# Kernel tuning notes

Measured on AMD Instinct MI355X. Metric: run time of the kernel, lower is better.

The kernel has to match this reference:

```python
import jax, jax.numpy as jnp
import numpy as np

B, T, D = 2, 2048, 1024
H, HD = 16, 64           # num_heads, head_dim (key_dim = value_dim = H*HD = D)
K = 4                    # short conv kernel size
EPS = 1e-6


def setup_inputs() -> dict:
    key = jax.random.key(0)
    ks = jax.random.split(key, 16)
    w = lambda k, shape, s=0.02: jax.random.normal(k, shape, jnp.float32) * s
    dt = jnp.exp(jax.random.uniform(ks[12], (H,)) * (np.log(0.1) - np.log(0.001)) + np.log(0.001))
    dt = jnp.clip(dt, 0.0001, None)
    return {
        "hidden_states": jax.random.normal(ks[0], (B, T, D), jnp.float32),
        "Wq": w(ks[1], (H * HD, D)),
        "Wk": w(ks[2], (H * HD, D)),
        "Wv": w(ks[3], (H * HD, D)),
        "Wa": w(ks[4], (H, D)),
        "Wb": w(ks[5], (H, D)),
        "Wg": w(ks[6], (H * HD, D)),
        "Wo": w(ks[7], (D, H * HD)),
        "q_norm_w": jnp.ones((HD,), jnp.float32),
        "k_norm_w": jnp.ones((HD,), jnp.float32),
        "o_norm_w": jnp.ones((HD,), jnp.float32),
        "A_log": jnp.log(jax.random.uniform(ks[11], (H,), jnp.float32, 0.5, 8.0)),
        "dt_bias": dt + jnp.log(-jnp.expm1(-dt)),
        "conv_q_w": w(ks[13], (H * HD, K), 0.2),
        "conv_k_w": w(ks[14], (H * HD, K), 0.2),
        "conv_v_w": w(ks[15], (H * HD, K), 0.2),
    }


def _short_conv_silu(x, w):
    # causal depthwise conv1d (kernel K) + SiLU; x: [B,T,C], w: [C,K]
    xc = jnp.transpose(x, (0, 2, 1))                       # [B,C,T]
    y = jax.lax.conv_general_dilated(
        xc, w[:, None, :], (1,), [(w.shape[-1] - 1, 0)],
        dimension_numbers=("NCH", "OIH", "NCH"), feature_group_count=w.shape[0])
    y = jnp.transpose(y, (0, 2, 1))
    return y * jax.nn.sigmoid(y)


def _rmsnorm(x, w):
    return x * jax.lax.rsqrt(jnp.mean(x * x, -1, keepdims=True) + EPS) * w


def _l2norm(x):
    return x * jax.lax.rsqrt(jnp.sum(x * x, -1, keepdims=True) + EPS)


def _forward(hidden_states, Wq, Wk, Wv, Wa, Wb, Wg, Wo,
             q_norm_w, k_norm_w, o_norm_w, A_log, dt_bias,
             conv_q_w, conv_k_w, conv_v_w):
    h = hidden_states
    q = _short_conv_silu(h @ Wq.T, conv_q_w).reshape(B, T, H, HD)
    k = _short_conv_silu(h @ Wk.T, conv_k_w).reshape(B, T, H, HD)
    v = _short_conv_silu(h @ Wv.T, conv_v_w).reshape(B, T, H, HD)
    q = _l2norm(_rmsnorm(q, q_norm_w))
    k = _l2norm(_rmsnorm(k, k_norm_w))
    beta = jax.nn.sigmoid(h @ Wb.T)                                  # [B,T,H]
    g = -jnp.exp(A_log) * jax.nn.softplus(h @ Wa.T + dt_bias)        # [B,T,H]
    scale = HD ** -0.5

    def step(S, inp):  # S: [B,H,dk,dv]
        qt, kt, vt, gt, bt = inp
        S = S * jnp.exp(gt)[:, :, None, None]
        kv = jnp.einsum("bhk,bhkv->bhv", kt, S)
        delta = (vt - kv) * bt[..., None]
        S = S + jnp.einsum("bhk,bhv->bhkv", kt, delta)
        o = jnp.einsum("bhk,bhkv->bhv", qt * scale, S)
        return S, o

    tm = lambda x: jnp.swapaxes(x, 0, 1)  # [B,T,...] -> [T,B,...]
    S0 = jnp.zeros((B, H, HD, HD), jnp.float32)
    _, o = jax.lax.scan(step, S0, (tm(q), tm(k), tm(v), tm(g), tm(beta)))
    o = jnp.swapaxes(o, 0, 1)                                        # [B,T,H,HD]

    gv = (h @ Wg.T).reshape(B, T, H, HD)
    o = _rmsnorm(o, o_norm_w) * (gv * jax.nn.sigmoid(gv))            # swish gate
    return o.reshape(B, T, H * HD) @ Wo.T


def reference(hidden_states, Wq, Wk, Wv, Wa, Wb, Wg, Wo,
              q_norm_w, k_norm_w, o_norm_w, A_log, dt_bias,
              conv_q_w, conv_k_w, conv_v_w):
    return _forward(hidden_states, Wq, Wk, Wv, Wa, Wb, Wg, Wo,
                    q_norm_w, k_norm_w, o_norm_w, A_log, dt_bias,
                    conv_q_w, conv_k_w, conv_v_w)
```

## Files before the change

### kernel.cpp

```cpp
#include <hip/hip_runtime.h>
#include <cstdint>
#include <cstddef>

#define B_ 2
#define T_ 2048
#define D_ 1024
#define H_ 16
#define HD_ 64
#define NC_ 32

typedef unsigned short u16;
typedef __attribute__((ext_vector_type(8))) short bf16x8;
typedef __attribute__((ext_vector_type(4))) float f32x4;

__device__ __forceinline__ float dot4(float4 a, float4 b, float acc) {
  return fmaf(a.x, b.x, fmaf(a.y, b.y, fmaf(a.z, b.z, fmaf(a.w, b.w, acc))));
}
__device__ __forceinline__ u16 f2bf(float f) {
  unsigned u = __float_as_uint(f);
  u += 0x7fffu + ((u >> 16) & 1u);
  return (u16)(u >> 16);
}
__device__ __forceinline__ float bf2f(u16 v) {
  return __uint_as_float(((unsigned)v) << 16);
}
__device__ __forceinline__ float4 ld4bf(const u16* p) {
  uint2 v = *(const uint2*)p;
  return float4{__uint_as_float(v.x << 16),
                __uint_as_float(v.x & 0xffff0000u),
                __uint_as_float(v.y << 16),
                __uint_as_float(v.y & 0xffff0000u)};
}
__device__ __forceinline__ bf16x8 pack8(float4 a, float4 b) {
  union { u16 us[8]; bf16x8 v; } p;
  p.us[0] = f2bf(a.x); p.us[1] = f2bf(a.y); p.us[2] = f2bf(a.z); p.us[3] = f2bf(a.w);
  p.us[4] = f2bf(b.x); p.us[5] = f2bf(b.y); p.us[6] = f2bf(b.z); p.us[7] = f2bf(b.w);
  return p.v;
}
__device__ __forceinline__ void glds16(const u16* g, u16* l) {
  __builtin_amdgcn_global_load_lds(
      (const __attribute__((address_space(1))) void*)g,
      (__attribute__((address_space(3))) void*)l, 16, 0, 0);
}
__device__ __forceinline__ float4 conv4(float4 x0, float4 x1, float4 x2, float4 x3,
                                        const float4* w) {
  float4 y;
  y.x = fmaf(w[0].x, x0.x, fmaf(w[0].y, x1.x, fmaf(w[0].z, x2.x, w[0].w * x3.x)));
  y.y = fmaf(w[1].x, x0.y, fmaf(w[1].y, x1.y, fmaf(w[1].z, x2.y, w[1].w * x3.y)));
  y.z = fmaf(w[2].x, x0.z, fmaf(w[2].y, x1.z, fmaf(w[2].z, x2.z, w[2].w * x3.z)));
  y.w = fmaf(w[3].x, x0.w, fmaf(w[3].y, x1.w, fmaf(w[3].z, x2.w, w[3].w * x3.w)));
  return y;
}
__device__ __forceinline__ float4 silu4(float4 a) {
  return float4{a.x / (1.f + __expf(-a.x)), a.y / (1.f + __expf(-a.y)),
                a.z / (1.f + __expf(-a.z)), a.w / (1.f + __expf(-a.w))};
}

__global__ __launch_bounds__(256) void cvt_all(
    const float* __restrict__ h, const float* __restrict__ w0,
    const float* __restrict__ w1, const float* __restrict__ w2,
    const float* __restrict__ w3, const float* __restrict__ w4,
    u16* __restrict__ h_bf, u16* __restrict__ wb)
{
  const int blk = blockIdx.x;
  const float* src;
  u16* dst;
  int lb;
  if (blk < 2048) { src = h; dst = h_bf; lb = blk; }
  else {
    int k = (blk - 2048) >> 9, r = (blk - 2048) & 511;
    src = k == 0 ? w0 : k == 1 ? w1 : k == 2 ? w2 : k == 3 ? w3 : w4;
    dst = wb + (size_t)k * 1048576;
    lb = r;
  }
  int i = (lb * 256 + threadIdx.x) * 8;
  float4 v0 = *(const float4*)(src + i);
  float4 v1 = *(const float4*)(src + i + 4);
  union { u16 us[8]; uint4 u4; } p;
  p.us[0] = f2bf(v0.x); p.us[1] = f2bf(v0.y); p.us[2] = f2bf(v0.z); p.us[3] = f2bf(v0.w);
  p.us[4] = f2bf(v1.x); p.us[5] = f2bf(v1.y); p.us[6] = f2bf(v1.z); p.us[7] = f2bf(v1.w);
  *(uint4*)(dst + i) = p.u4;
}

__global__ __launch_bounds__(512, 1) void gemm_bf16_4(const u16* __restrict__ A,
    const u16* __restrict__ W0, const u16* __restrict__ W1,
    const u16* __restrict__ W2, const u16* __restrict__ W3,
    u16* __restrict__ C0, u16* __restrict__ C1,
    u16* __restrict__ C2, u16* __restrict__ C3)
{
  __shared__ u16 As[3 * 256 * 32];
  __shared__ u16 Bs[3 * 256 * 32];
  const int K = 1024, N = 1024;
  const int sel = blockIdx.y >> 2;
  const u16* Bw = sel == 0 ? W0 : sel == 1 ? W1 : sel == 2 ? W2 : W3;
  u16* C = sel == 0 ? C0 : sel == 1 ? C1 : sel == 2 ? C2 : C3;
  const int row0 = blockIdx.x * 256;
  const int col0 = (blockIdx.y & 3) * 256;
  const int tid = threadIdx.x;
  const int lane = tid & 63, wave = tid >> 6;
  const int wm = wave >> 2, wn = wave & 3;
  const int lr = lane & 15, lkq = lane >> 4;
  const int lkp = (lkq ^ ((lr >> 1) & 3)) * 8;

  f32x4 acc[8][4];
  #pragma unroll
  for (int i = 0; i < 8; ++i)
    #pragma unroll
    for (int j = 0; j < 4; ++j) acc[i][j] = f32x4{0.f, 0.f, 0.f, 0.f};

  auto STAGE = [&](int buf, int kt) {
    u16* ab = As + buf * 8192;
    u16* bb = Bs + buf * 8192;
    #pragma unroll
    for (int g = 0; g < 2; ++g) {
      const int idx = g * 512 + tid;
      const int rr = idx >> 2, cl = idx & 3;
      const int csw = (cl ^ ((rr >> 1) & 3)) * 8;
      glds16(A  + (size_t)(row0 + rr) * K + kt * 32 + csw, ab + idx * 8);
      glds16(Bw + (size_t)(col0 + rr) * K + kt * 32 + csw, bb + idx * 8);
    }
  };

  const int KT = K >> 5;
  STAGE(0, 0); STAGE(1, 1); STAGE(2, 2);
  asm volatile("s_waitcnt vmcnt(8)" ::: "memory");
  __builtin_amdgcn_s_barrier();
  __builtin_amdgcn_sched_barrier(0);

  for (int kt = 0; kt < KT; ++kt) {
    const int cur = kt % 3;
    const u16* Asc = As + cur * 8192;
    const u16* Bsc = Bs + cur * 8192;
    bf16x8 af[8], bfr[4];
    #pragma unroll
    for (int i = 0; i < 8; ++i)
      af[i] = *(const bf16x8*)&Asc[(wm * 128 + i * 16 + lr) * 32 + lkp];
    #pragma unroll
    for (int j = 0; j < 4; ++j)
      bfr[j] = *(const bf16x8*)&Bsc[(wn * 64 + j * 16 + lr) * 32 + lkp];
    __builtin_amdgcn_s_setprio(1);
    #pragma unroll
    for (int i = 0; i < 4; ++i)
      #pragma unroll
      for (int j = 0; j < 4; ++j)
        acc[i][j] = __builtin_amdgcn_mfma_f32_16x16x32_bf16(af[i], bfr[j], acc[i][j], 0, 0, 0);
    __builtin_amdgcn_s_setprio(0);
    asm volatile("s_waitcnt lgkmcnt(0)" ::: "memory");
    __builtin_amdgcn_sched_barrier(0);
    __builtin_amdgcn_s_barrier();
    __builtin_amdgcn_sched_barrier(0);
    if (kt + 3 < KT) {
      STAGE(cur, kt + 3);
      asm volatile("s_waitcnt vmcnt(4)" ::: "memory");
    } else {
      asm volatile("s_waitcnt vmcnt(0)" ::: "memory");
    }
    __builtin_amdgcn_s_setprio(1);
    #pragma unroll
    for (int i = 4; i < 8; ++i)
      #pragma unroll
      for (int j = 0; j < 4; ++j)
        acc[i][j] = __builtin_amdgcn_mfma_f32_16x16x32_bf16(af[i], bfr[j], acc[i][j], 0, 0, 0);
    __builtin_amdgcn_s_setprio(0);
    __builtin_amdgcn_sched_barrier(0);
    __builtin_amdgcn_s_barrier();
    __builtin_amdgcn_sched_barrier(0);
  }

  const int orow = row0 + wm * 128 + (lane >> 4) * 4;
  const int ocol = col0 + wn * 64 + lr;
  #pragma unroll
  for (int i = 0; i < 8; ++i)
    #pragma unroll
    for (int j = 0; j < 4; ++j)
      #pragma unroll
      for (int r = 0; r < 4; ++r)
        C[(size_t)(orow + i * 16 + r) * N + ocol + j * 16] = f2bf(acc[i][j][r]);
}

__device__ __forceinline__ void gemm_core128(const u16* __restrict__ A,
    const u16* __restrict__ Bw, float* __restrict__ C,
    u16* As, u16* Bs, int row0, int col0, int K, int N)
{
  const int tid = threadIdx.x;
  const int lane = tid & 63, wave = tid >> 6;
  const int wr = (wave >> 1) * 64, wc = (wave & 1) * 64;
  const int lr = lane & 15;
  const int lkp = (((lane >> 4) ^ ((lr >> 1) & 3))) * 8;
  const int rql = (lane >> 2);
  const int cql = (((lane & 3) ^ ((rql >> 1) & 3))) * 8;
  const u16* gA0 = A + (size_t)(row0 + wave * 16 + rql) * K + cql;
  const u16* gA1 = A + (size_t)(row0 + (wave + 4) * 16 + rql) * K + cql;
  const u16* gB0 = Bw + (size_t)(col0 + wave * 16 + rql) * K + cql;
  const u16* gB1 = Bw + (size_t)(col0 + (wave + 4) * 16 + rql) * K + cql;

  f32x4 acc[4][4];
  #pragma unroll
  for (int i = 0; i < 4; ++i)
    #pragma unroll
    for (int j = 0; j < 4; ++j) acc[i][j] = f32x4{0.f, 0.f, 0.f, 0.f};

  auto STAGE = [&](int buf, int kt) {
    u16* ab = As + buf * 4096;
    u16* bb = Bs + buf * 4096;
    glds16(gA0 + kt * 32, ab + wave * 512);
    glds16(gA1 + kt * 32, ab + (wave + 4) * 512);
    glds16(gB0 + kt * 32, bb + wave * 512);
    glds16(gB1 + kt * 32, bb + (wave + 4) * 512);
  };

  const int KT = K >> 5;
  STAGE(0, 0);
  STAGE(1, 1);
  int cur = 0;
  for (int kt = 0; kt < KT; ++kt) {
    if (kt + 2 < KT) {
      STAGE(cur == 0 ? 2 : (cur == 1 ? 0 : 1), kt + 2);
      asm volatile("s_waitcnt vmcnt(8)" ::: "memory");
    } else if (kt + 1 < KT) {
      asm volatile("s_waitcnt vmcnt(4)" ::: "memory");
    } else {
      asm volatile("s_waitcnt vmcnt(0)" ::: "memory");
    }
    __builtin_amdgcn_s_barrier();
    __builtin_amdgcn_sched_barrier(0);
    const u16* Asc = As + cur * 4096;
    const u16* Bsc = Bs + cur * 4096;
    bf16x8 af[4], bf[4];
    #pragma unroll
    for (int i = 0; i < 4; ++i) af[i] = *(const bf16x8*)&Asc[(wr + i * 16 + lr) * 32 + lkp];
    #pragma unroll
    for (int j = 0; j < 4; ++j) bf[j] = *(const bf16x8*)&Bsc[(wc + j * 16 + lr) * 32 + lkp];
    #pragma unroll
    for (int i = 0; i < 4; ++i)
      #pragma unroll
      for (int j = 0; j < 4; ++j)
        acc[i][j] = __builtin_amdgcn_mfma_f32_16x16x32_bf16(af[i], bf[j], acc[i][j], 0, 0, 0);
    __builtin_amdgcn_sched_barrier(0);
    __builtin_amdgcn_s_barrier();
    cur = (cur == 2) ? 0 : cur + 1;
  }
  const int orow = row0 + wr + (lane >> 4) * 4;
  const int ocol = col0 + wc + lr;
  #pragma unroll
  for (int i = 0; i < 4; ++i)
    #pragma unroll
    for (int j = 0; j < 4; ++j)
      #pragma unroll
      for (int r = 0; r < 4; ++r)
        C[(size_t)(orow + i * 16 + r) * N + ocol + j * 16] = acc[i][j][r];
}

__global__ __launch_bounds__(256) void gemm_bf16_1(const u16* __restrict__ A,
    const u16* __restrict__ Bw, float* __restrict__ C)
{
  __shared__ u16 As[3 * 128 * 32];
  __shared__ u16 Bs[3 * 128 * 32];
  gemm_core128(A, Bw, C, As, Bs, blockIdx.x * 128, blockIdx.y * 128, 1024, 1024);
}

#define SPW 261
__global__ __launch_bounds__(256) void smallproj(const float* __restrict__ Hs,
    const float* __restrict__ Wa, const float* __restrict__ Wb,
    const float* __restrict__ Alog, const float* __restrict__ dtb,
    float* __restrict__ Gout, float* __restrict__ Bout)
{
  __shared__ float hT[16][SPW];
  __shared__ float wT[32][SPW];
  const int row0 = blockIdx.x * 16;
  const int tid = threadIdx.x;
  const int r = tid >> 5;
  const int c = tid & 31;
  float a0 = 0.f, a1 = 0.f;
  for (int kc = 0; kc < 4; ++kc) {
    const int k0 = kc * 256;
    #pragma unroll
    for (int i = 0; i < 4; ++i) {
      int e4 = tid + i * 256;
      int rr = e4 >> 6, k4 = (e4 & 63) * 4;
      *(float4*)&hT[rr][k4] = *(const float4*)&Hs[(size_t)(row0 + rr) * D_ + k0 + k4];
    }
    #pragma unroll
    for (int i = 0; i < 8; ++i) {
      int e4 = tid + i * 256;
      int rr = e4 >> 6, k4 = (e4 & 63) * 4;
      const float* wsrc = (rr < 16) ? (Wa + (size_t)rr * D_) : (Wb + (size_t)(rr - 16) * D_);
      *(float4*)&wT[rr][k4] = *(const float4*)&wsrc[k0 + k4];
    }
    __syncthreads();
    #pragma unroll 8
    for (int k = 0; k < 256; k += 4) {
      float4 wv = *(const float4*)&wT[c][k];
      float4 h0 = *(const float4*)&hT[r][k];
      float4 h1 = *(const float4*)&hT[r + 8][k];
      a0 = dot4(h0, wv, a0);
      a1 = dot4(h1, wv, a1);
    }
    __syncthreads();
  }
  if (c < 16) {
    const float al = -__expf(Alog[c]);
    const float db = dtb[c];
    float x0 = a0 + db, x1 = a1 + db;
    float sp0 = fmaxf(x0, 0.f) + log1pf(__expf(-fabsf(x0)));
    float sp1 = fmaxf(x1, 0.f) + log1pf(__expf(-fabsf(x1)));
    Gout[(size_t)(row0 + r) * H_ + c] = al * sp0;
    Gout[(size_t)(row0 + r + 8) * H_ + c] = al * sp1;
  } else {
    const int hd = c - 16;
    Bout[(size_t)(row0 + r) * H_ + hd] = 1.f / (1.f + __expf(-a0));
    Bout[(size_t)(row0 + r + 8) * H_ + hd] = 1.f / (1.f + __expf(-a1));
  }
}

__global__ __launch_bounds__(256) void p1_chunk(
    const u16* __restrict__ Kp, const u16* __restrict__ Vp,
    const float* __restrict__ Gg, const float* __restrict__ Bb,
    const float* __restrict__ ckw, const float* __restrict__ cvw,
    const float* __restrict__ knw,
    u16* __restrict__ Ubf, u16* __restrict__ Wbf, u16* __restrict__ Kcb,
    float* __restrict__ Gcum, float* __restrict__ Mbuf, float* __restrict__ Nbuf)
{
  __shared__ u16 Kbf[64][72];
  __shared__ float Am[64][68];
  __shared__ float XT[128][68];
  __shared__ float gc[64], bet[64];
  const int bhc = blockIdx.x;
  const int bh = bhc >> 5, c = bhc & 31;
  const int b = bh >> 4, h = bh & 15;
  const int tid = threadIdx.x;
  const int lane = tid & 63, wave = tid >> 6;
  const int lr = lane & 15, lkq = lane >> 4;
  const size_t rowbase = ((size_t)b*T_ + c*64)*H_ + h;
  const int c4 = (tid & 15) * 4;
  const int hh64 = h * 64;

  if (tid < 64) {
    float gv = Gg[rowbase + (size_t)tid*H_];
    #pragma unroll
    for (int off = 1; off < 64; off <<= 1) {
      float up = __shfl_up(gv, off, 64);
      if (tid >= off) gv += up;
    }
    gc[tid] = gv;
    Gcum[(size_t)bhc*64 + tid] = gv;
    bet[tid] = Bb[rowbase + (size_t)tid*H_];
  }

  {
    float4 wk[4];
    float nwv[4];
    #pragma unroll
    for (int cc = 0; cc < 4; ++cc) {
      wk[cc] = *(const float4*)(ckw + (hh64 + c4 + cc) * 4);
      nwv[cc] = knw[c4 + cc];
    }
    #pragma unroll
    for (int k = 0; k < 4; ++k) {
      const int t = (tid >> 4) + k * 16;
      const int gt = c * 64 + t;
      const u16* src = Kp + (rowbase + (size_t)t * H_) * 64 + c4;
      float4 x3 = ld4bf(src);
      float4 x2 = (gt >= 1) ? ld4bf(src - D_)   : float4{0,0,0,0};
      float4 x1 = (gt >= 2) ? ld4bf(src - 2*D_) : float4{0,0,0,0};
      float4 x0 = (gt >= 3) ? ld4bf(src - 3*D_) : float4{0,0,0,0};
      float4 y = silu4(conv4(x0, x1, x2, x3, wk));
      float ss = fmaf(y.x, y.x, fmaf(y.y, y.y, fmaf(y.z, y.z, y.w * y.w)));
      ss += __shfl_xor(ss, 1); ss += __shfl_xor(ss, 2);
      ss += __shfl_xor(ss, 4); ss += __shfl_xor(ss, 8);
      const float inv1 = rsqrtf(ss * (1.f/64.f) + 1e-6f);
      float4 z = {y.x*inv1*nwv[0], y.y*inv1*nwv[1], y.z*inv1*nwv[2], y.w*inv1*nwv[3]};
      float s2 = fmaf(z.x, z.x, fmaf(z.y, z.y, fmaf(z.z, z.z, z.w * z.w)));
      s2 += __shfl_xor(s2, 1); s2 += __shfl_xor(s2, 2);
      s2 += __shfl_xor(s2, 4); s2 += __shfl_xor(s2, 8);
      const float inv2 = rsqrtf(s2 + 1e-6f);
      u16 tmp[4] = {f2bf(z.x*inv2), f2bf(z.y*inv2), f2bf(z.z*inv2), f2bf(z.w*inv2)};
      *(uint2*)&Kbf[t][c4] = *(uint2*)tmp;
      *(uint2*)&Kcb[(size_t)bhc*4096 + (size_t)t*64 + c4] = *(uint2*)tmp;
    }
  }
  __syncthreads();

  {
    bf16x8 afA[2];
    #pragma unroll
    for (int ks = 0; ks < 2; ++ks)
      afA[ks] = *(const bf16x8*)&Kbf[16*wave + lr][ks*32 + lkq*8];
    __builtin_amdgcn_s_setprio(1);
    #pragma unroll
    for (int j = 0; j < 4; ++j) {
      f32x4 accA = f32x4{0.f, 0.f, 0.f, 0.f};
      #pragma unroll
      for (int ks = 0; ks < 2; ++ks) {
        bf16x8 bfr = *(const bf16x8*)&Kbf[16*j + lr][ks*32 + lkq*8];
        accA = __builtin_amdgcn_mfma_f32_16x16x32_bf16(afA[ks], bfr, accA, 0, 0, 0);
      }
      const int s = 16*j + lr;
      #pragma unroll
      for (int r = 0; r < 4; ++r) {
        int t = 16*wave + lkq*4 + r;
        Am[t][s] = (s < t) ? bet[t] * __expf(gc[t] - gc[s]) * accA[r] : 0.f;
      }
    }
    __builtin_amdgcn_s_setprio(0);
  }
  {
    float4 wv[4];
    #pragma unroll
    for (int cc = 0; cc < 4; ++cc)
      wv[cc] = *(const float4*)(cvw + (hh64 + c4 + cc) * 4);
    #pragma unroll
    for (int k = 0; k < 4; ++k) {
      const int t = (tid >> 4) + k * 16;
      const int gt = c * 64 + t;
      const u16* src = Vp + (rowbase + (size_t)t * H_) * 64 + c4;
      float4 x3 = ld4bf(src);
      float4 x2 = (gt >= 1) ? ld4bf(src - D_)   : float4{0,0,0,0};
      float4 x1 = (gt >= 2) ? ld4bf(src - 2*D_) : float4{0,0,0,0};
      float4 x0 = (gt >= 3) ? ld4bf(src - 3*D_) : float4{0,0,0,0};
      float4 vv = silu4(conv4(x0, x1, x2, x3, wv));
      const float bt = bet[t];
      const float ek = bt * __expf(gc[t]);
      XT[c4+0][t] = bt * vv.x; XT[c4+1][t] = bt * vv.y;
      XT[c4+2][t] = bt * vv.z; XT[c4+3][t] = bt * vv.w;
      XT[64+c4+0][t] = ek * bf2f(Kbf[t][c4+0]);
      XT[64+c4+1][t] = ek * bf2f(Kbf[t][c4+1]);
      XT[64+c4+2][t] = ek * bf2f(Kbf[t][c4+2]);
      XT[64+c4+3][t] = ek * bf2f(Kbf[t][c4+3]);
    }
  }
  __syncthreads();

  for (int st = 0; st < 4; ++st) {
    if (st > 0) {
      const int nks = (st == 3) ? 2 : 1;
      f32x4 accU0 = f32x4{0.f,0.f,0.f,0.f}, accU1 = f32x4{0.f,0.f,0.f,0.f};
      __builtin_amdgcn_s_setprio(1);
      for (int ks = 0; ks < nks; ++ks) {
        const int m0 = ks*32 + lkq*8;
        bf16x8 af;
        if (m0 + 8 <= 16*st) {
          float4 a0 = *(const float4*)&Am[16*st + lr][m0];
          float4 a1 = *(const float4*)&Am[16*st + lr][m0 + 4];
          af = pack8(a0, a1);
        } else {
          af = bf16x8{0,0,0,0,0,0,0,0};
        }
        {
          const int cb = (wave*2 + 0) * 16;
          float4 b0 = *(const float4*)&XT[cb + lr][m0];
          float4 b1 = *(const float4*)&XT[cb + lr][m0 + 4];
          accU0 = __builtin_amdgcn_mfma_f32_16x16x32_bf16(af, pack8(b0, b1), accU0, 0, 0, 0);
        }
        {
          const int cb = (wave*2 + 1) * 16;
          float4 b0 = *(const float4*)&XT[cb + lr][m0];
          float4 b1 = *(const float4*)&XT[cb + lr][m0 + 4];
          accU1 = __builtin_amdgcn_mfma_f32_16x16x32_bf16(af, pack8(b0, b1), accU1, 0, 0, 0);
        }
      }
      __builtin_amdgcn_s_setprio(0);
      #pragma unroll
      for (int r = 0; r < 4; ++r) {
        const int t = 16*st + lkq*4 + r;
        XT[(wave*2+0)*16 + lr][t] -= accU0[r];
        XT[(wave*2+1)*16 + lr][t] -= accU1[r];
      }
      __syncthreads();
    }
    if (tid < 128) {
      const int bs = 16*st;
      float x[16];
      #pragma unroll
      for (int q = 0; q < 4; ++q)
        *(float4*)&x[q*4] = *(const float4*)&XT[tid][bs + q*4];
      #pragma unroll
      for (int tau = 1; tau < 16; ++tau) {
        float a = 0.f, a2 = 0.f;
        #pragma unroll
        for (int m = 0; m < tau; m += 2) {
          a = fmaf(Am[bs+tau][bs+m], x[m], a);
          if (m + 1 < tau) a2 = fmaf(Am[bs+tau][bs+m+1], x[m+1], a2);
        }
        x[tau] -= (a + a2);
      }
      #pragma unroll
      for (int q = 0; q < 4; ++q)
        *(float4*)&XT[tid][bs + q*4] = *(const float4*)&x[q*4];
    }
    __syncthreads();
  }

  for (int e = tid; e < 4096; e += 256) {
    int t = e >> 6, j = e & 63;
    Ubf[(size_t)bhc*4096 + e] = f2bf(XT[j][t]);
    Wbf[(size_t)bhc*4096 + e] = f2bf(XT[64+j][t]);
  }

  u16* KTb = (u16*)&Am[0][0];
  if (tid < 64) bet[tid] = __expf(gc[63] - gc[tid]);
  __syncthreads();
  for (int e4 = tid; e4 < 1024; e4 += 256) {
    int t = e4 >> 4, a4 = (e4 & 15) * 4;
    u16 k0 = Kbf[t][a4+0], k1 = Kbf[t][a4+1], k2 = Kbf[t][a4+2], k3 = Kbf[t][a4+3];
    KTb[(a4+0)*72 + t] = k0;
    KTb[(a4+1)*72 + t] = k1;
    KTb[(a4+2)*72 + t] = k2;
    KTb[(a4+3)*72 + t] = k3;
  }
  __syncthreads();

  bf16x8 afK[2];
  #pragma unroll
  for (int ks = 0; ks < 2; ++ks)
    afK[ks] = *(const bf16x8*)&KTb[(16*wave + lr)*72 + ks*32 + lkq*8];
  const float bC = __expf(gc[63]);
  const size_t ob = (size_t)bhc * 4096;
  #pragma unroll
  for (int j = 0; j < 4; ++j) {
    f32x4 aM = f32x4{0.f,0.f,0.f,0.f}, aN = f32x4{0.f,0.f,0.f,0.f};
    __builtin_amdgcn_s_setprio(1);
    #pragma unroll
    for (int ks = 0; ks < 2; ++ks) {
      const int m0 = ks*32 + lkq*8;
      float4 sc0 = *(const float4*)&bet[m0];
      float4 sc1 = *(const float4*)&bet[m0 + 4];
      float4 w0 = *(const float4*)&XT[64 + 16*j + lr][m0];
      float4 w1 = *(const float4*)&XT[64 + 16*j + lr][m0 + 4];
      float4 u0 = *(const float4*)&XT[16*j + lr][m0];
      float4 u1 = *(const float4*)&XT[16*j + lr][m0 + 4];
      w0.x*=sc0.x; w0.y*=sc0.y; w0.z*=sc0.z; w0.w*=sc0.w;
      w1.x*=sc1.x; w1.y*=sc1.y; w1.z*=sc1.z; w1.w*=sc1.w;
      u0.x*=sc0.x; u0.y*=sc0.y; u0.z*=sc0.z; u0.w*=sc0.w;
      u1.x*=sc1.x; u1.y*=sc1.y; u1.z*=sc1.z; u1.w*=sc1.w;
      aM = __builtin_amdgcn_mfma_f32_16x16x32_bf16(afK[ks], pack8(w0, w1), aM, 0, 0, 0);
      aN = __builtin_amdgcn_mfma_f32_16x16x32_bf16(afK[ks], pack8(u0, u1), aN, 0, 0, 0);
    }
    __builtin_amdgcn_s_setprio(0);
    const int cc = 16*j + lr;
    #pragma unroll
    for (int r = 0; r < 4; ++r) {
      const int a = 16*wave + lkq*4 + r;
      Mbuf[ob + (size_t)a*64 + cc] = (a == cc ? bC : 0.f) - aM[r];
      Nbuf[ob + (size_t)a*64 + cc] = aN[r];
    }
  }
}

__global__ __launch_bounds__(256) void pscanA(float* __restrict__ Mbuf,
    float* __restrict__ Nbuf)
{
  __shared__ float OM[2][64][68];
  __shared__ float ON[2][64][68];
  __shared__ float NM[2][64][68];
  const int blk = blockIdx.x;
  const int bh = blk >> 3, g = blk & 7;
  const size_t s0 = ((size_t)bh * 32 + g * 4) * 4096;
  const int tid = threadIdx.x;
  const int p0 = (tid >> 4) * 4;
  const int q0 = (tid & 15) * 4;
  for (int e4 = tid; e4 < 1024; e4 += 256) {
    int r = e4 >> 4, c4 = (e4 & 15) * 4;
    *(float4*)&OM[0][r][c4] = *(const float4*)&Mbuf[s0 + (size_t)r*64 + c4];
    *(float4*)&ON[0][r][c4] = *(const float4*)&Nbuf[s0 + (size_t)r*64 + c4];
    *(float4*)&NM[0][r][c4] = *(const float4*)&Mbuf[s0 + 4096 + (size_t)r*64 + c4];
  }
  __syncthreads();
  for (int s = 0; s < 3; ++s) {
    const int cur = s & 1, nxt = cur ^ 1;
    const size_t wslot = s0 + (size_t)(s + 1) * 4096;
    if (s < 2) {
      for (int e4 = tid; e4 < 1024; e4 += 256) {
        int r = e4 >> 4, c4 = (e4 & 15) * 4;
        *(float4*)&NM[nxt][r][c4] = *(const float4*)&Mbuf[wslot + 4096 + (size_t)r*64 + c4];
      }
    }
    float aM[4][4], aN[4][4];
    #pragma unroll
    for (int r = 0; r < 4; ++r) {
      float4 nv = *(const float4*)&Nbuf[wslot + (size_t)(p0+r)*64 + q0];
      aM[r][0]=0.f; aM[r][1]=0.f; aM[r][2]=0.f; aM[r][3]=0.f;
      aN[r][0]=nv.x; aN[r][1]=nv.y; aN[r][2]=nv.z; aN[r][3]=nv.w;
    }
    for (int m4 = 0; m4 < 64; m4 += 4) {
      float xv[4][4];
      #pragma unroll
      for (int r = 0; r < 4; ++r) {
        float4 v = *(const float4*)&NM[cur][p0+r][m4];
        xv[r][0]=v.x; xv[r][1]=v.y; xv[r][2]=v.z; xv[r][3]=v.w;
      }
      #pragma unroll
      for (int mm = 0; mm < 4; ++mm) {
        float4 ym = *(const float4*)&OM[cur][m4+mm][q0];
        float4 yn = *(const float4*)&ON[cur][m4+mm][q0];
        #pragma unroll
        for (int r = 0; r < 4; ++r) {
          aM[r][0] = fmaf(xv[r][mm], ym.x, aM[r][0]);
          aM[r][1] = fmaf(xv[r][mm], ym.y, aM[r][1]);
          aM[r][2] = fmaf(xv[r][mm], ym.z, aM[r][2]);
          aM[r][3] = fmaf(xv[r][mm], ym.w, aM[r][3]);
          aN[r][0] = fmaf(xv[r][mm], yn.x, aN[r][0]);
          aN[r][1] = fmaf(xv[r][mm], yn.y, aN[r][1]);
          aN[r][2] = fmaf(xv[r][mm], yn.z, aN[r][2]);
          aN[r][3] = fmaf(xv[r][mm], yn.w, aN[r][3]);
        }
      }
    }
    #pragma unroll
    for (int r = 0; r < 4; ++r) {
      float4 vm = {aM[r][0], aM[r][1], aM[r][2], aM[r][3]};
      float4 vn = {aN[r][0], aN[r][1], aN[r][2], aN[r][3]};
      *(float4*)&Mbuf[wslot + (size_t)(p0+r)*64 + q0] = vm;
      *(float4*)&Nbuf[wslot + (size_t)(p0+r)*64 + q0] = vn;
      *(float4*)&OM[nxt][p0+r][q0] = vm;
      *(float4*)&ON[nxt][p0+r][q0] = vn;
    }
    __syncthreads();
  }
}

__global__ __launch_bounds__(256) void pscanB(const float* __restrict__ Mbuf,
    const float* __restrict__ Nbuf, float* __restrict__ S0b)
{
  __shared__ float ST[2][64][68];
  __shared__ float MT[64][68];
  const int bh = blockIdx.x;
  const size_t base = (size_t)bh * 32 * 4096;
  const int tid = threadIdx.x;
  const int j0 = (tid >> 4) * 4, a0 = tid & 15;
  for (int e4 = tid; e4 < 1024; e4 += 256) {
    int r = e4 >> 4, c4 = (e4 & 15) * 4;
    *(float4*)&ST[0][r][c4] = float4{0.f, 0.f, 0.f, 0.f};
    *(float4*)&S0b[base + (size_t)r*64 + c4] = float4{0.f, 0.f, 0.f, 0.f};
  }
  for (int g = 0; g < 7; ++g) {
    const int cur = g & 1, nxt = cur ^ 1;
    const size_t tslot = base + (size_t)(4*g + 3) * 4096;
    for (int e4 = tid; e4 < 1024; e4 += 256) {
      int r = e4 >> 4, c4 = (e4 & 15) * 4;
      *(float4*)&MT[r][c4] = *(const float4*)&Mbuf[tslot + (size_t)r*64 + c4];
    }
    float acc[4][4];
    #pragma unroll
    for (int r = 0; r < 4; ++r)
      #pragma unroll
      for (int s = 0; s < 4; ++s)
        acc[r][s] = Nbuf[tslot + (size_t)(a0 + 16*s)*64 + j0 + r];
    __syncthreads();
    for (int k4 = 0; k4 < 64; k4 += 4) {
      float4 xr[4];
      #pragma unroll
      for (int r = 0; r < 4; ++r) xr[r] = *(const float4*)&ST[cur][j0+r][k4];
      #pragma unroll
      for (int s = 0; s < 4; ++s) {
        float4 yv = *(const float4*)&MT[a0 + 16*s][k4];
        #pragma unroll
        for (int r = 0; r < 4; ++r) acc[r][s] = dot4(xr[r], yv, acc[r][s]);
      }
    }
    const size_t oslot = base + (size_t)(4*(g+1)) * 4096;
    #pragma unroll
    for (int r = 0; r < 4; ++r)
      #pragma unroll
      for (int s = 0; s < 4; ++s) {
        ST[nxt][j0+r][a0 + 16*s] = acc[r][s];
        S0b[oslot + (size_t)(j0+r)*64 + a0 + 16*s] = acc[r][s];
      }
    __syncthreads();
  }
}

__global__ __launch_bounds__(256) void p3_out(
    const u16* __restrict__ Qp, const u16* __restrict__ Kcb,
    const float* __restrict__ cqw, const float* __restrict__ qnw,
    const float* __restrict__ Gcum, const float* __restrict__ S0b,
    const float* __restrict__ Mbuf, const float* __restrict__ Nbuf,
    const u16* __restrict__ Ubf, const u16* __restrict__ Wbfg,
    const u16* __restrict__ GV, const float* __restrict__ onw,
    u16* __restrict__ OG)
{
  __shared__ u16 Qbf[64][72];
  __shared__ u16 Kbf[64][72];
  __shared__ u16 S0T[64][72];
  __shared__ u16 Wbf[64][72];
  __shared__ u16 Pbf[64][72];
  __shared__ u16 DsT[64][72];
  __shared__ float gcs[64];
  __shared__ float onws[64];
  const int bhc = blockIdx.x;
  const int bh = bhc >> 5, c = bhc & 31;
  const int b = bh >> 4, h = bh & 15;
  const int tid = threadIdx.x;
  const int lane = tid & 63, wave = tid >> 6;
  const int lr = lane & 15, lkq = lane >> 4;
  const size_t rowbase = ((size_t)b*T_ + c*64)*H_ + h;
  const int c4 = (tid & 15) * 4;
  const int hh64 = h * 64;
  const int ii = c & 3;
  if (tid < 64) { gcs[tid] = Gcum[(size_t)bhc*64 + tid]; onws[tid] = onw[tid]; }

  {
    float4 wq[4];
    float nwv[4];
    #pragma unroll
    for (int cc = 0; cc < 4; ++cc) {
      wq[cc] = *(const float4*)(cqw + (hh64 + c4 + cc) * 4);
      nwv[cc] = qnw[c4 + cc];
    }
    #pragma unroll
    for (int k = 0; k < 4; ++k) {
      const int t = (tid >> 4) + k * 16;
      const int gt = c * 64 + t;
      const u16* src = Qp + (rowbase + (size_t)t * H_) * 64 + c4;
      float4 x3 = ld4bf(src);
      float4 x2 = (gt >= 1) ? ld4bf(src - D_)   : float4{0,0,0,0};
      float4 x1 = (gt >= 2) ? ld4bf(src - 2*D_) : float4{0,0,0,0};
      float4 x0 = (gt >= 3) ? ld4bf(src - 3*D_) : float4{0,0,0,0};
      float4 y = silu4(conv4(x0, x1, x2, x3, wq));
      float ss = fmaf(y.x, y.x, fmaf(y.y, y.y, fmaf(y.z, y.z, y.w * y.w)));
      ss += __shfl_xor(ss, 1); ss += __shfl_xor(ss, 2);
      ss += __shfl_xor(ss, 4); ss += __shfl_xor(ss, 8);
      const float inv1 = rsqrtf(ss * (1.f/64.f) + 1e-6f);
      float4 z = {y.x*inv1*nwv[0], y.y*inv1*nwv[1], y.z*inv1*nwv[2], y.w*inv1*nwv[3]};
      float s2 = fmaf(z.x, z.x, fmaf(z.y, z.y, fmaf(z.z, z.z, z.w * z.w)));
      s2 += __shfl_xor(s2, 1); s2 += __shfl_xor(s2, 2);
      s2 += __shfl_xor(s2, 4); s2 += __shfl_xor(s2, 8);
      const float inv2 = rsqrtf(s2 + 1e-6f) * 0.125f;
      u16 tmp[4] = {f2bf(z.x*inv2), f2bf(z.y*inv2), f2bf(z.z*inv2), f2bf(z.w*inv2)};
      *(uint2*)&Qbf[t][c4] = *(uint2*)tmp;
    }
  }
  for (int e4 = tid; e4 < 1024; e4 += 256) {
    int t = e4 >> 4, d4 = (e4 & 15) * 4;
    *(uint2*)&Kbf[t][d4] = *(const uint2*)&Kcb[(size_t)bhc*4096 + (size_t)t*64 + d4];
    *(uint2*)&Wbf[t][d4] = *(const uint2*)&Wbfg[(size_t)bhc*4096 + (size_t)t*64 + d4];
  }
  if (ii == 0) {
    for (int e4 = tid; e4 < 1024; e4 += 256) {
      int t = e4 >> 4, d4 = (e4 & 15) * 4;
      float4 sv = *(const float4*)&S0b[(size_t)bhc*4096 + (size_t)t*64 + d4];
      u16 as[4] = {f2bf(sv.x), f2bf(sv.y), f2bf(sv.z), f2bf(sv.w)};
      *(uint2*)&S0T[t][d4] = *(uint2*)as;
    }
  } else {
    const size_t gslot = ((size_t)bh*NC_ + (c & ~3)) * 4096;
    const size_t pslot = ((size_t)bh*NC_ + c - 1) * 4096;
    for (int e4 = tid; e4 < 1024; e4 += 256) {
      int t = e4 >> 4, d4 = (e4 & 15) * 4;
      float4 sg = *(const float4*)&S0b[gslot + (size_t)t*64 + d4];
      float4 mp = *(const float4*)&Mbuf[pslot + (size_t)t*64 + d4];
      u16 a1[4] = {f2bf(sg.x), f2bf(sg.y), f2bf(sg.z), f2bf(sg.w)};
      u16 a2[4] = {f2bf(mp.x), f2bf(mp.y), f2bf(mp.z), f2bf(mp.w)};
      *(uint2*)&DsT[t][d4] = *(uint2*)a1;
      *(uint2*)&Pbf[t][d4] = *(uint2*)a2;
    }
  }
  __syncthreads();

  if (ii != 0) {
    const size_t pslot = ((size_t)bh*NC_ + c - 1) * 4096;
    bf16x8 ag[2];
    #pragma unroll
    for (int ks = 0; ks < 2; ++ks)
      ag[ks] = *(const bf16x8*)&DsT[16*wave + lr][ks*32 + lkq*8];
    #pragma unroll
    for (int ab = 0; ab < 4; ++ab) {
      f32x4 cin;
      {
        float4 nv = *(const float4*)&Nbuf[pslot + (size_t)(16*ab + lr)*64 + 16*wave + lkq*4];
        cin[0] = nv.x; cin[1] = nv.y; cin[2] = nv.z; cin[3] = nv.w;
      }
      __builtin_amdgcn_s_setprio(1);
      #pragma unroll
      for (int ks = 0; ks < 2; ++ks) {
        bf16x8 bm = *(const bf16x8*)&Pbf[16*ab + lr][ks*32 + lkq*8];
        cin = __builtin_amdgcn_mfma_f32_16x16x32_bf16(ag[ks], bm, cin, 0, 0, 0);
      }
      __builtin_amdgcn_s_setprio(0);
      #pragma unroll
      for (int r = 0; r < 4; ++r)
        S0T[16*wave + lkq*4 + r][16*ab + lr] = f2bf(cin[r]);
    }
    __syncthreads();
  }

  const int trow0 = 16*wave + lkq*4;
  bf16x8 aq[2], aw[2];
  #pragma unroll
  for (int ks = 0; ks < 2; ++ks) {
    aq[ks] = *(const bf16x8*)&Qbf[16*wave + lr][ks*32 + lkq*8];
    aw[ks] = *(const bf16x8*)&Wbf[16*wave + lr][ks*32 + lkq*8];
  }
  float gct[4], egt[4];
  #pragma unroll
  for (int r = 0; r < 4; ++r) { gct[r] = gcs[trow0 + r]; egt[r] = __expf(gct[r]); }

  #pragma unroll
  for (int j = 0; j < 4; ++j) {
    f32x4 pa = f32x4{0.f,0.f,0.f,0.f};
    __builtin_amdgcn_s_setprio(1);
    #pragma unroll
    for (int ks = 0; ks < 2; ++ks) {
      bf16x8 bk = *(const bf16x8*)&Kbf[16*j + lr][ks*32 + lkq*8];
      pa = __builtin_amdgcn_mfma_f32_16x16x32_bf16(aq[ks], bk, pa, 0, 0, 0);
    }
    __builtin_amdgcn_s_setprio(0);
    const int s = 16*j + lr;
    const float gs = gcs[s];
    #pragma unroll
    for (int r = 0; r < 4; ++r) {
      const int t = trow0 + r;
      float val = (s <= t) ? __expf(gct[r] - gs) * pa[r] : 0.f;
      Pbf[t][s] = f2bf(val);
    }
  }

  #pragma unroll
  for (int j = 0; j < 4; ++j) {
    f32x4 da = f32x4{0.f,0.f,0.f,0.f};
    __builtin_amdgcn_s_setprio(1);
    #pragma unroll
    for (int ks = 0; ks < 2; ++ks) {
      bf16x8 bs = *(const bf16x8*)&S0T[16*j + lr][ks*32 + lkq*8];
      da = __builtin_amdgcn_mfma_f32_16x16x32_bf16(aw[ks], bs, da, 0, 0, 0);
    }
    __builtin_amdgcn_s_setprio(0);
    const int jj = 16*j + lr;
    #pragma unroll
    for (int r = 0; r < 4; ++r) {
      const int s = trow0 + r;
      float dv = bf2f(Ubf[(size_t)bhc*4096 + (size_t)s*64 + jj]) - da[r];
      DsT[jj][s] = f2bf(dv);
    }
  }

  f32x4 oacc[4];
  #pragma unroll
  for (int j = 0; j < 4; ++j) {
    f32x4 oa = f32x4{0.f,0.f,0.f,0.f};
    __builtin_amdgcn_s_setprio(1);
    #pragma unroll
    for (int ks = 0; ks < 2; ++ks) {
      bf16x8 bs = *(const bf16x8*)&S0T[16*j + lr][ks*32 + lkq*8];
      oa = __builtin_amdgcn_mfma_f32_16x16x32_bf16(aq[ks], bs, oa, 0, 0, 0);
    }
    __builtin_amdgcn_s_setprio(0);
    #pragma unroll
    for (int r = 0; r < 4; ++r) oa[r] *= egt[r];
    oacc[j] = oa;
  }
  __syncthreads();

  bf16x8 ap[2];
  #pragma unroll
  for (int ks = 0; ks < 2; ++ks)
    ap[ks] = *(const bf16x8*)&Pbf[16*wave + lr][ks*32 + lkq*8];
  __builtin_amdgcn_s_setprio(1);
  #pragma unroll
  for (int j = 0; j < 4; ++j) {
    #pragma unroll
    for (int ks = 0; ks < 2; ++ks) {
      bf16x8 bd = *(const bf16x8*)&DsT[16*j + lr][ks*32 + lkq*8];
      oacc[j] = __builtin_amdgcn_mfma_f32_16x16x32_bf16(ap[ks], bd, oacc[j], 0, 0, 0);
    }
  }
  __builtin_amdgcn_s_setprio(0);

  #pragma unroll
  for (int r = 0; r < 4; ++r) {
    float ss = 0.f;
    #pragma unroll
    for (int jq = 0; jq < 4; ++jq) ss = fmaf(oacc[jq][r], oacc[jq][r], ss);
    ss += __shfl_xor(ss, 1); ss += __shfl_xor(ss, 2);
    ss += __shfl_xor(ss, 4); ss += __shfl_xor(ss, 8);
    const float inv = rsqrtf(ss * (1.f/64.f) + 1e-6f);
    const int t = trow0 + r;
    const size_t rowoff = ((size_t)b*T_ + (size_t)c*64 + t) * D_ + h*64;
    #pragma unroll
    for (int jq = 0; jq < 4; ++jq) {
      const int jj = 16*jq + lr;
      float y = oacc[jq][r] * inv * onws[jj];
      float gv = bf2f(GV[rowoff + jj]);
      OG[rowoff + jj] = f2bf(y * gv / (1.f + __expf(-gv)));
    }
  }
}

extern "C" void kernel_launch(void* const* d_in, const int* in_sizes, int n_in,
                              void* d_out, int out_size, void* d_ws, size_t ws_size,
                              hipStream_t stream) {
  const float* h    = (const float*)d_in[0];
  const float* Wq   = (const float*)d_in[1];
  const float* Wk   = (const float*)d_in[2];
  const float* Wv   = (const float*)d_in[3];
  const float* Wa   = (const float*)d_in[4];
  const float* Wb   = (const float*)d_in[5];
  const float* Wg   = (const float*)d_in[6];
  const float* Wo   = (const float*)d_in[7];
  const float* qnw  = (const float*)d_in[8];
  const float* knw  = (const float*)d_in[9];
  const float* onw  = (const float*)d_in[10];
  const float* Alog = (const float*)d_in[11];
  const float* dtb  = (const float*)d_in[12];
  const float* cqw  = (const float*)d_in[13];
  const float* ckw  = (const float*)d_in[14];
  const float* cvw  = (const float*)d_in[15];
  float* out = (float*)d_out;
  float* ws  = (float*)d_ws;

  const size_t NB = (size_t)B_ * T_ * D_;
  float* qp   = ws;
  float* kp   = ws + 1*NB;
  float* vp   = ws + 2*NB;
  float* gvp  = ws + 3*NB;
  float* qc   = ws + 4*NB;
  float* kc   = ws + 5*NB;
  float* vc   = ws + 6*NB;
  float* mb   = ws + 7*NB;
  float* wbf  = ws + 8*NB;
  float* gb   = ws + 8*NB + 5*524288;
  float* bb   = gb + (size_t)B_*T_*H_;
  float* Gc   = bb + (size_t)B_*T_*H_;

  u16* h_bf  = (u16*)mb;
  u16* og_bf = (u16*)kp;
  u16* w_bf  = (u16*)wbf;
  u16* wq_bf = w_bf + 0*1048576;
  u16* wk_bf = w_bf + 1*1048576;
  u16* wv_bf = w_bf + 2*1048576;
  u16* wg_bf = w_bf + 3*1048576;
  u16* wo_bf = w_bf + 4*1048576;

  u16*   Qpb  = (u16*)qp;
  u16*   Kpb  = (u16*)kp;
  u16*   Vpb  = (u16*)vp;
  u16*   GVb  = (u16*)gvp;
  u16*   Ubf  = (u16*)qc;
  u16*   Wbfp = (u16*)qc + NB;
  u16*   Kcb  = (u16*)kc;
  float* Nbuf = vc;
  float* S0b  = vp;
  float* Mbuf = mb;

  cvt_all<<<4608, 256, 0, stream>>>(h, Wq, Wk, Wv, Wg, Wo, h_bf, w_bf);

  gemm_bf16_4<<<dim3(16, 16), 512, 0, stream>>>(h_bf, wq_bf, wk_bf, wv_bf, wg_bf,
                                                 Qpb, Kpb, Vpb, GVb);
  smallproj<<<256, 256, 0, stream>>>(h, Wa, Wb, Alog, dtb, gb, bb);

  p1_chunk<<<B_*H_*NC_, 256, 0, stream>>>(Kpb, Vpb, gb, bb, ckw, cvw, knw,
                                          Ubf, Wbfp, Kcb, Gc, Mbuf, Nbuf);
  pscanA<<<B_*H_*8, 256, 0, stream>>>(Mbuf, Nbuf);
  pscanB<<<B_*H_, 256, 0, stream>>>(Mbuf, Nbuf, S0b);
  p3_out<<<B_*H_*NC_, 256, 0, stream>>>(Qpb, Kcb, cqw, qnw, Gc, S0b, Mbuf, Nbuf,
                                        Ubf, Wbfp, GVb, onw, og_bf);

  gemm_bf16_1<<<dim3(32, 8), 256, 0, stream>>>(og_bf, wo_bf, out);
}
```

Measured before the change: 215.5 us.

## Restructure fused QKVG GEMM into double-buffered 64-wide K tiles with staggered loads

Replaces the triple-buffered 32-wide K pipeline of the 4-way projection GEMM with a double-buffered layout holding 64-wide K tiles (two 32-wide sub-slices per buffer). Global-to-LDS loads for the next tile are split into quarters and interleaved between four MFMA phases, with A fragments read in two halves to lower register pressure. The goal is to halve the loop trip count and hide load latency behind compute more evenly. In exchange it adds more barriers per iteration and uses about the same LDS (128KB versus 96KB).

```diff
diff --git a/kernel.cpp b/kernel.cpp
--- a/kernel.cpp
+++ b/kernel.cpp
@@ -88,9 +88,8 @@
     u16* __restrict__ C0, u16* __restrict__ C1,
     u16* __restrict__ C2, u16* __restrict__ C3)
 {
-  __shared__ u16 As[3 * 256 * 32];
-  __shared__ u16 Bs[3 * 256 * 32];
-  const int K = 1024, N = 1024;
+  __shared__ u16 L[2 * 32768];
+  const int K = 1024, N = 1024, KT = 16;
   const int sel = blockIdx.y >> 2;
   const u16* Bw = sel == 0 ? W0 : sel == 1 ? W1 : sel == 2 ? W2 : W3;
   u16* C = sel == 0 ? C0 : sel == 1 ? C1 : sel == 2 ? C2 : C3;
@@ -100,7 +99,8 @@
   const int lane = tid & 63, wave = tid >> 6;
   const int wm = wave >> 2, wn = wave & 3;
   const int lr = lane & 15, lkq = lane >> 4;
-  const int lkp = (lkq ^ ((lr >> 1) & 3)) * 8;
+  const int rr = tid >> 2, cl = tid & 3;
+  const int csw = (cl ^ ((rr >> 1) & 3)) * 8;
 
   f32x4 acc[8][4];
   #pragma unroll
@@ -108,63 +108,103 @@
     #pragma unroll
     for (int j = 0; j < 4; ++j) acc[i][j] = f32x4{0.f, 0.f, 0.f, 0.f};
 
-  auto STAGE = [&](int buf, int kt) {
-    u16* ab = As + buf * 8192;
-    u16* bb = Bs + buf * 8192;
-    #pragma unroll
-    for (int g = 0; g < 2; ++g) {
-      const int idx = g * 512 + tid;
-      const int rr = idx >> 2, cl = idx & 3;
-      const int csw = (cl ^ ((rr >> 1) & 3)) * 8;
-      glds16(A  + (size_t)(row0 + rr) * K + kt * 32 + csw, ab + idx * 8);
-      glds16(Bw + (size_t)(col0 + rr) * K + kt * 32 + csw, bb + idx * 8);
-    }
+  auto STAGEU = [&](int buf, int kt, const u16* src, int matOfs, int baseRow, int ks, int rh) {
+    glds16(src + (size_t)(baseRow + rh * 128 + rr) * K + kt * 64 + ks * 32 + csw,
+           L + buf * 32768 + matOfs + ks * 8192 + rh * 4096 + tid * 8);
   };
-
-  const int KT = K >> 5;
-  STAGE(0, 0); STAGE(1, 1); STAGE(2, 2);
-  asm volatile("s_waitcnt vmcnt(8)" ::: "memory");
+  auto rdA = [&](int buf, int ks, int ih, bf16x8* af) {
+    #pragma unroll
+    for (int i = 0; i < 4; ++i) {
+      const int R = wm * 128 + (ih * 4 + i) * 16 + lr;
+      af[i] = *(const bf16x8*)&L[buf * 32768 + ks * 8192 + R * 32 + ((lkq ^ ((R >> 1) & 3)) * 8)];
+    }
+  };
+  auto rdB = [&](int buf, int ks, bf16x8* bf) {
+    #pragma unroll
+    for (int j = 0; j < 4; ++j) {
+      const int R = wn * 64 + j * 16 + lr;
+      bf[j] = *(const bf16x8*)&L[buf * 32768 + 16384 + ks * 8192 + R * 32 + ((lkq ^ ((R >> 1) & 3)) * 8)];
+    }
+  };
+
+  STAGEU(0, 0, A, 0, row0, 0, 0);  STAGEU(0, 0, A, 0, row0, 0, 1);
+  STAGEU(0, 0, Bw, 16384, col0, 0, 0); STAGEU(0, 0, Bw, 16384, col0, 0, 1);
+  STAGEU(0, 0, A, 0, row0, 1, 0);  STAGEU(0, 0, A, 0, row0, 1, 1);
+  STAGEU(0, 0, Bw, 16384, col0, 1, 0); STAGEU(0, 0, Bw, 16384, col0, 1, 1);
+  asm volatile("s_waitcnt vmcnt(4)" ::: "memory");
   __builtin_amdgcn_s_barrier();
   __builtin_amdgcn_sched_barrier(0);
 
   for (int kt = 0; kt < KT; ++kt) {
-    const int cur = kt % 3;
-    const u16* Asc = As + cur * 8192;
-    const u16* Bsc = Bs + cur * 8192;
-    bf16x8 af[8], bfr[4];
-    #pragma unroll
-    for (int i = 0; i < 8; ++i)
-      af[i] = *(const bf16x8*)&Asc[(wm * 128 + i * 16 + lr) * 32 + lkp];
-    #pragma unroll
-    for (int j = 0; j < 4; ++j)
-      bfr[j] = *(const bf16x8*)&Bsc[(wn * 64 + j * 16 + lr) * 32 + lkp];
-    __builtin_amdgcn_s_setprio(1);
-    #pragma unroll
-    for (int i = 0; i < 4; ++i)
-      #pragma unroll
-      for (int j = 0; j < 4; ++j)
-        acc[i][j] = __builtin_amdgcn_mfma_f32_16x16x32_bf16(af[i], bfr[j], acc[i][j], 0, 0, 0);
-    __builtin_amdgcn_s_setprio(0);
+    const int cb = kt & 1, nb = cb ^ 1;
+    const bool st = (kt + 1 < KT);
+    bf16x8 af[4], bfr[4];
+    rdB(cb, 0, bfr);
+    rdA(cb, 0, 0, af);
+    if (st) { STAGEU(nb, kt + 1, A, 0, row0, 0, 0); STAGEU(nb, kt + 1, A, 0, row0, 0, 1); }
+    __builtin_amdgcn_s_barrier();
     asm volatile("s_waitcnt lgkmcnt(0)" ::: "memory");
     __builtin_amdgcn_sched_barrier(0);
-    __builtin_amdgcn_s_barrier();
-    __builtin_amdgcn_sched_barrier(0);
-    if (kt + 3 < KT) {
-      STAGE(cur, kt + 3);
-      asm volatile("s_waitcnt vmcnt(4)" ::: "memory");
-    } else {
-      asm volatile("s_waitcnt vmcnt(0)" ::: "memory");
-    }
     __builtin_amdgcn_s_setprio(1);
     #pragma unroll
-    for (int i = 4; i < 8; ++i)
+    for (int i = 0; i < 4; ++i)
       #pragma unroll
       for (int j = 0; j < 4; ++j)
         acc[i][j] = __builtin_amdgcn_mfma_f32_16x16x32_bf16(af[i], bfr[j], acc[i][j], 0, 0, 0);
     __builtin_amdgcn_s_setprio(0);
     __builtin_amdgcn_sched_barrier(0);
     __builtin_amdgcn_s_barrier();
+    rdA(cb, 0, 1, af);
+    if (st) { STAGEU(nb, kt + 1, Bw, 16384, col0, 0, 0); STAGEU(nb, kt + 1, Bw, 16384, col0, 0, 1); }
+    if (kt == KT - 1) {
+      asm volatile("s_waitcnt vmcnt(0)" ::: "memory");
+    } else {
+      asm volatile("s_waitcnt vmcnt(4)" ::: "memory");
+    }
+    __builtin_amdgcn_s_barrier();
+    asm volatile("s_waitcnt lgkmcnt(0)" ::: "memory");
     __builtin_amdgcn_sched_barrier(0);
+    __builtin_amdgcn_s_setprio(1);
+    #pragma unroll
+    for (int i = 0; i < 4; ++i)
+      #pragma unroll
+      for (int j = 0; j < 4; ++j)
+        acc[4 + i][j] = __builtin_amdgcn_mfma_f32_16x16x32_bf16(af[i], bfr[j], acc[4 + i][j], 0, 0, 0);
+    __builtin_amdgcn_s_setprio(0);
+    __builtin_amdgcn_sched_barrier(0);
+    __builtin_amdgcn_s_barrier();
+    rdB(cb, 1, bfr);
+    rdA(cb, 1, 0, af);
+    if (st) { STAGEU(nb, kt + 1, A, 0, row0, 1, 0); STAGEU(nb, kt + 1, A, 0, row0, 1, 1); }
+    __builtin_amdgcn_s_barrier();
+    asm volatile("s_waitcnt lgkmcnt(0)" ::: "memory");
+    __builtin_amdgcn_sched_barrier(0);
+    __builtin_amdgcn_s_setprio(1);
+    #pragma unroll
+    for (int i = 0; i < 4; ++i)
+      #pragma unroll
+      for (int j = 0; j < 4; ++j)
+        acc[i][j] = __builtin_amdgcn_mfma_f32_16x16x32_bf16(af[i], bfr[j], acc[i][j], 0, 0, 0);
+    __builtin_amdgcn_s_setprio(0);
+    __builtin_amdgcn_sched_barrier(0);
+    __builtin_amdgcn_s_barrier();
+    rdA(cb, 1, 1, af);
+    if (st) {
+      STAGEU(nb, kt + 1, Bw, 16384, col0, 1, 0); STAGEU(nb, kt + 1, Bw, 16384, col0, 1, 1);
+      asm volatile("s_waitcnt vmcnt(4)" ::: "memory");
+    }
+    __builtin_amdgcn_s_barrier();
+    asm volatile("s_waitcnt lgkmcnt(0)" ::: "memory");
+    __builtin_amdgcn_sched_barrier(0);
+    __builtin_amdgcn_s_setprio(1);
+    #pragma unroll
+    for (int i = 0; i < 4; ++i)
+      #pragma unroll
+      for (int j = 0; j < 4; ++j)
+        acc[4 + i][j] = __builtin_amdgcn_mfma_f32_16x16x32_bf16(af[i], bfr[j], acc[4 + i][j], 0, 0, 0);
+    __builtin_amdgcn_s_setprio(0);
+    __builtin_amdgcn_sched_barrier(0);
+    __builtin_amdgcn_s_barrier();
   }
 
   const int orow = row0 + wm * 128 + (lane >> 4) * 4;
```

New measurement: 214.2 us. Within noise of the previous version (-0.6%).
